# Kernel tuning notes

Hardware: AMD Instinct MI355X
Metric: run time of the kernel (lower is better)

## Reference

```python
import jax, jax.numpy as jnp
import numpy as np

B, L, D, H, FF = 8, 512, 1024, 16, 1024
HD = D // H
EPS = 1e-5
ROPE_BASE = 10000.0
ROPE_DIM = D  # module passes dim=embed_dim (not head_dim) to RotaryPositionalEmbeddings


def _layer_norm(x, g, b):
    m = jnp.mean(x, axis=-1, keepdims=True)
    v = jnp.var(x, axis=-1, keepdims=True)
    return (x - m) * jax.lax.rsqrt(v + EPS) * g + b


def _rope(x):
    # x: [B, H, L, HD]; interleaved-pair rotation, frequencies base**(-2i/ROPE_DIM)
    half = HD // 2
    inv_freq = 1.0 / (ROPE_BASE ** (jnp.arange(half, dtype=jnp.float32) * 2.0 / ROPE_DIM))
    ang = jnp.arange(L, dtype=jnp.float32)[:, None] * inv_freq[None, :]  # [L, half]
    cos = jnp.cos(ang)
    sin = jnp.sin(ang)
    xr = x.reshape(*x.shape[:-1], half, 2)
    x1, x2 = xr[..., 0], xr[..., 1]
    out = jnp.stack([x1 * cos - x2 * sin, x1 * sin + x2 * cos], axis=-1)
    return out.reshape(x.shape).astype(x.dtype)


def setup_inputs() -> dict:
    key = jax.random.key(0)
    ks = jax.random.split(key, 16)
    sd = 0.02
    n = lambda k, shape: (jax.random.normal(k, shape, dtype=jnp.float32) * sd)
    return {
        "input_ids": jax.random.normal(ks[0], (B, L, D), dtype=jnp.float32),
        "Wq": n(ks[1], (FF, D)), "bq": jnp.zeros((D,), jnp.float32),
        "Wk": n(ks[2], (FF, D)), "bk": jnp.zeros((D,), jnp.float32),
        "Wv": n(ks[3], (FF, D)), "bv": jnp.zeros((D,), jnp.float32),
        "Wo": n(ks[4], (D, D)),  "bo": jnp.zeros((D,), jnp.float32),
        "Wf": n(ks[5], (D, FF)), "bf": jnp.zeros((FF,), jnp.float32),
        "g_ffn": jnp.ones((D,), jnp.float32), "b_ffn": jnp.zeros((D,), jnp.float32),
        "g_attn": jnp.ones((FF,), jnp.float32), "b_attn": jnp.zeros((FF,), jnp.float32),
    }


def reference(input_ids, Wq, bq, Wk, bk, Wv, bv, Wo, bo, Wf, bf,
              g_ffn, b_ffn, g_attn, b_attn):
    # FFN branch: computed then DISCARDED in the original source (x is overwritten).
    _ffn_dead = jax.nn.relu(_layer_norm(input_ids, g_ffn, b_ffn) @ Wf + bf)  # noqa: F841

    x = _layer_norm(input_ids, g_attn, b_attn)  # pre_attn_norm applied to input_ids
    q = (x @ Wq + bq).reshape(B, L, H, HD).transpose(0, 2, 1, 3)  # [B,H,L,HD]
    k = (x @ Wk + bk).reshape(B, L, H, HD).transpose(0, 2, 1, 3)
    v = (x @ Wv + bv).reshape(B, L, H, HD).transpose(0, 2, 1, 3)
    q = _rope(q)
    k = _rope(k)

    scale = 1.0 / np.sqrt(HD).astype(np.float32)
    scores = jnp.einsum("bhqd,bhkd->bhqk", q, k) * scale  # [B,H,L,L]
    attn = jax.nn.softmax(scores, axis=-1)
    o = jnp.einsum("bhqk,bhkd->bhqd", attn, v)
    o = o.transpose(0, 2, 1, 3).reshape(B, L, D)
    return input_ids + (o @ Wo + bo)
```

## Files before the change

### kernel.cpp

```cpp
#include <hip/hip_runtime.h>

typedef unsigned short ushort_t;
typedef short bf16x8 __attribute__((ext_vector_type(8)));
typedef float f32x4 __attribute__((ext_vector_type(4)));

#define B_ 8
#define L_ 512
#define D_ 1024
#define H_ 16
#define M_ 4096

__device__ __forceinline__ ushort_t f2bf(float f) {
  union { float f; unsigned u; } v; v.f = f;
  unsigned r = v.u + 0x7FFFu + ((v.u >> 16) & 1u);
  return (ushort_t)(r >> 16);
}

__device__ __forceinline__ void gl_lds16(const ushort_t* g, ushort_t* s) {
  __builtin_amdgcn_global_load_lds((const __attribute__((address_space(1))) void*)(g),
                                   (__attribute__((address_space(3))) void*)(s), 16, 0, 0);
}

__global__ __launch_bounds__(256) void prep_kernel(const float* __restrict__ x,
                                                   const float* __restrict__ g,
                                                   const float* __restrict__ b,
                                                   ushort_t* __restrict__ xn,
                                                   float2* __restrict__ csb,
                                                   const float* __restrict__ w0,
                                                   const float* __restrict__ w1,
                                                   const float* __restrict__ w2,
                                                   const float* __restrict__ w3,
                                                   ushort_t* __restrict__ wt) {
  __shared__ float tile[32][33];
  int blk = blockIdx.x, t = threadIdx.x;
  if (blk < 1024) {
    int row = blk * 4 + (t >> 6);
    int lane = t & 63;
    const float4* xr = (const float4*)(x + (size_t)row * D_);
    float4 v[4];
    float s = 0.f, s2 = 0.f;
#pragma unroll
    for (int j = 0; j < 4; ++j) {
      v[j] = xr[j * 64 + lane];
      s  += v[j].x + v[j].y + v[j].z + v[j].w;
      s2 += v[j].x * v[j].x + v[j].y * v[j].y + v[j].z * v[j].z + v[j].w * v[j].w;
    }
#pragma unroll
    for (int m = 1; m < 64; m <<= 1) { s += __shfl_xor(s, m); s2 += __shfl_xor(s2, m); }
    float mean = s * (1.0f / D_);
    float var  = s2 * (1.0f / D_) - mean * mean;
    float rs   = rsqrtf(var + 1e-5f);
    unsigned long long* outp = (unsigned long long*)(xn + (size_t)row * D_);
#pragma unroll
    for (int j = 0; j < 4; ++j) {
      float4 gg = ((const float4*)g)[j * 64 + lane];
      float4 bb = ((const float4*)b)[j * 64 + lane];
      unsigned long long pk =
          (unsigned long long)f2bf((v[j].x - mean) * rs * gg.x + bb.x)
        | ((unsigned long long)f2bf((v[j].y - mean) * rs * gg.y + bb.y) << 16)
        | ((unsigned long long)f2bf((v[j].z - mean) * rs * gg.z + bb.z) << 32)
        | ((unsigned long long)f2bf((v[j].w - mean) * rs * gg.w + bb.w) << 48);
      outp[j * 64 + lane] = pk;
    }
  } else if (blk < 1088) {
    int idx = (blk - 1024) * 256 + t;
    int l = idx >> 5, i = idx & 31;
    float inv = powf(10000.0f, (-2.0f * (float)i) / 1024.0f);
    float ang = (float)l * inv;
    csb[idx] = make_float2(cosf(ang), sinf(ang));
  } else {
    int wb = blk - 1088;
    int z = wb >> 10;
    const float* W = (z == 0) ? w0 : (z == 1) ? w1 : (z == 2) ? w2 : w3;
    ushort_t* WT = wt + ((size_t)z << 20);
    int rem = wb & 1023;
    int by = rem >> 5, bx = rem & 31;
    int tx = t & 31, ty = t >> 5;
    int k0 = by * 32, n0 = bx * 32;
#pragma unroll
    for (int j = 0; j < 4; ++j)
      tile[ty + 8 * j][tx] = W[(size_t)(k0 + ty + 8 * j) * 1024 + n0 + tx];
    __syncthreads();
#pragma unroll
    for (int j = 0; j < 4; ++j)
      WT[(size_t)(n0 + ty + 8 * j) * 1024 + k0 + tx] = f2bf(tile[tx][ty + 8 * j]);
  }
}

__global__ __launch_bounds__(256) void gemm_qkv_kernel(const ushort_t* __restrict__ xn,
                                                       const ushort_t* __restrict__ wt,
                                                       const float* __restrict__ bq,
                                                       const float* __restrict__ bk,
                                                       const float* __restrict__ bv,
                                                       ushort_t* __restrict__ qb,
                                                       ushort_t* __restrict__ kb,
                                                       ushort_t* __restrict__ vt,
                                                       const float2* __restrict__ csb) {
  __shared__ ushort_t As[64 * 64];
  __shared__ ushort_t Bs[128 * 64];
  int t = threadIdx.x, l = t & 63, w = t >> 6, lr = l & 15, lg = l >> 4;
  int hid = blockIdx.x;
  int xcd = hid & 7, lid = hid >> 3;
  int by = (xcd >> 1) * 16 + lid / 12;
  int bx = (xcd & 1) * 12 + lid % 12;
  int m0 = by * 64;
  int n0g = bx * 128;
  int z = n0g >> 10;
  int n0 = n0g & 1023;
  const float* bias = (z == 0) ? bq : (z == 1) ? bk : bv;
  int wr = w >> 1, wc = w & 1;
  const int sr8 = l >> 3;
  const int scol = ((l & 7) ^ sr8) * 8;

  f32x4 acc[2][4] = {};

  for (int k0 = 0; k0 < 1024; k0 += 64) {
    gl_lds16(&xn[(size_t)(m0 + w * 16 + sr8) * 1024 + k0 + scol], &As[(w * 16) * 64]);
    gl_lds16(&xn[(size_t)(m0 + w * 16 + 8 + sr8) * 1024 + k0 + scol], &As[(w * 16 + 8) * 64]);
    gl_lds16(&wt[(size_t)(n0g + w * 32 + sr8) * 1024 + k0 + scol], &Bs[(w * 32) * 64]);
    gl_lds16(&wt[(size_t)(n0g + w * 32 + 8 + sr8) * 1024 + k0 + scol], &Bs[(w * 32 + 8) * 64]);
    gl_lds16(&wt[(size_t)(n0g + w * 32 + 16 + sr8) * 1024 + k0 + scol], &Bs[(w * 32 + 16) * 64]);
    gl_lds16(&wt[(size_t)(n0g + w * 32 + 24 + sr8) * 1024 + k0 + scol], &Bs[(w * 32 + 24) * 64]);
    __syncthreads();
#pragma unroll
    for (int kk = 0; kk < 2; ++kk) {
      bf16x8 a[2], bfr[4];
#pragma unroll
      for (int mi = 0; mi < 2; ++mi)
        a[mi] = *(const bf16x8*)&As[(wr * 32 + mi * 16 + lr) * 64 + (((kk * 4 + lg) ^ (lr & 7)) << 3)];
#pragma unroll
      for (int ni = 0; ni < 4; ++ni)
        bfr[ni] = *(const bf16x8*)&Bs[(wc * 64 + ni * 16 + lr) * 64 + (((kk * 4 + lg) ^ (lr & 7)) << 3)];
#pragma unroll
      for (int mi = 0; mi < 2; ++mi)
#pragma unroll
        for (int ni = 0; ni < 4; ++ni)
          acc[mi][ni] = __builtin_amdgcn_mfma_f32_16x16x32_bf16(a[mi], bfr[ni], acc[mi][ni], 0, 0, 0);
    }
    __syncthreads();
  }

  if (z < 2) {
    ushort_t* outp = (z == 0) ? qb : kb;
    const float sc = (z == 0) ? 0.18033688f : 1.0f;
#pragma unroll
    for (int mi = 0; mi < 2; ++mi) {
      int rowb = m0 + wr * 32 + mi * 16 + lg * 4;
#pragma unroll
      for (int ni = 0; ni < 4; ++ni) {
        int col = n0 + wc * 64 + ni * 16 + lr;
        float bvv = bias[col];
        int ii = (col & 63) >> 1;
        int codd = col & 1;
#pragma unroll
        for (int r = 0; r < 4; ++r) {
          float val = acc[mi][ni][r] + bvv;
          float par = __shfl_xor(val, 1);
          float2 cs = csb[((rowb + r) & 511) * 32 + ii];
          float y = codd ? (par * cs.y + val * cs.x) : (val * cs.x - par * cs.y);
          outp[(size_t)(rowb + r) * 1024 + col] = f2bf(y * sc);
        }
      }
    }
  } else {
#pragma unroll
    for (int mi = 0; mi < 2; ++mi) {
      int rowb = m0 + wr * 32 + mi * 16 + lg * 4;
      int bidx = rowb >> 9, l0 = rowb & 511;
#pragma unroll
      for (int ni = 0; ni < 4; ++ni) {
        int col = n0 + wc * 64 + ni * 16 + lr;
        float bvv = bias[col];
        unsigned long long pk =
            (unsigned long long)f2bf(acc[mi][ni][0] + bvv)
          | ((unsigned long long)f2bf(acc[mi][ni][1] + bvv) << 16)
          | ((unsigned long long)f2bf(acc[mi][ni][2] + bvv) << 32)
          | ((unsigned long long)f2bf(acc[mi][ni][3] + bvv) << 48);
        *(unsigned long long*)&vt[((size_t)(bidx << 10) + col) * 512 + l0] = pk;
      }
    }
  }
}

__global__ __launch_bounds__(256) void gemm_o_kernel(const ushort_t* __restrict__ A,
                                                     const ushort_t* __restrict__ Bt,
                                                     const float* __restrict__ bias,
                                                     const float* __restrict__ res,
                                                     float* __restrict__ out) {
  __shared__ ushort_t As[64 * 64];
  __shared__ ushort_t Bs[128 * 64];
  int t = threadIdx.x, l = t & 63, w = t >> 6, lr = l & 15, lg = l >> 4;
  int hid = blockIdx.x;
  int lid = (hid & 7) * 64 + (hid >> 3);
  int bx = lid & 7, by = lid >> 3;
  int m0 = by * 64, n0 = bx * 128;
  int wr = w >> 1, wc = w & 1;
  const int srow = l >> 3;
  const int scol = ((l & 7) ^ (srow & 7)) * 8;

  f32x4 acc[2][4] = {};

  for (int k0 = 0; k0 < 1024; k0 += 64) {
#pragma unroll
    for (int i = 0; i < 2; ++i)
      gl_lds16(&A[(size_t)(m0 + w * 16 + i * 8 + srow) * 1024 + k0 + scol],
               &As[(w * 16 + i * 8) * 64]);
#pragma unroll
    for (int i = 0; i < 4; ++i)
      gl_lds16(&Bt[(size_t)(n0 + w * 32 + i * 8 + srow) * 1024 + k0 + scol],
               &Bs[(w * 32 + i * 8) * 64]);
    __syncthreads();
#pragma unroll
    for (int kk = 0; kk < 2; ++kk) {
      bf16x8 a[2], bfr[4];
#pragma unroll
      for (int mi = 0; mi < 2; ++mi)
        a[mi] = *(const bf16x8*)&As[(wr * 32 + mi * 16 + lr) * 64 + (((kk * 4 + lg) ^ (lr & 7)) << 3)];
#pragma unroll
      for (int ni = 0; ni < 4; ++ni)
        bfr[ni] = *(const bf16x8*)&Bs[(wc * 64 + ni * 16 + lr) * 64 + (((kk * 4 + lg) ^ (lr & 7)) << 3)];
#pragma unroll
      for (int mi = 0; mi < 2; ++mi)
#pragma unroll
        for (int ni = 0; ni < 4; ++ni)
          acc[mi][ni] = __builtin_amdgcn_mfma_f32_16x16x32_bf16(a[mi], bfr[ni], acc[mi][ni], 0, 0, 0);
    }
    __syncthreads();
  }

#pragma unroll
  for (int mi = 0; mi < 2; ++mi) {
    int rowb = m0 + wr * 32 + mi * 16 + lg * 4;
#pragma unroll
    for (int ni = 0; ni < 4; ++ni) {
      int col = n0 + wc * 64 + ni * 16 + lr;
      float bvv = bias[col];
#pragma unroll
      for (int r = 0; r < 4; ++r) {
        size_t off = (size_t)(rowb + r) * 1024 + col;
        out[off] = acc[mi][ni][r] + bvv + res[off];
      }
    }
  }
}

__global__ __launch_bounds__(256) void attn_kernel(const ushort_t* __restrict__ q,
                                                   const ushort_t* __restrict__ k,
                                                   const ushort_t* __restrict__ vt,
                                                   ushort_t* __restrict__ o) {
  __shared__ ushort_t Ks[2][64 * 64];
  __shared__ ushort_t Vs[2][64 * 64];
  __shared__ ushort_t Ps[4][2][16 * 64];
  int t = threadIdx.x, l = t & 63, w = t >> 6, lr = l & 15, lg = l >> 4;
  int blk = blockIdx.x;
  int bh = blk & 127, qt = blk >> 7;
  int b = bh >> 4, h = bh & 15;
  const int srow = l >> 3;
  const int scol = ((l & 7) ^ (srow & 7)) * 8;

  bf16x8 qf[2][2];
#pragma unroll
  for (int qm = 0; qm < 2; ++qm) {
    size_t qrow = (size_t)(b * 512 + qt * 128 + w * 32 + qm * 16 + lr);
#pragma unroll
    for (int kh = 0; kh < 2; ++kh)
      qf[qm][kh] = *(const bf16x8*)&q[qrow * 1024 + h * 64 + kh * 32 + lg * 8];
  }

  f32x4 oacc[2][4] = {};
  float lrun[2] = {0.f, 0.f};

#define STAGE(buf, kv0)                                                              \
  {                                                                                  \
    _Pragma("unroll")                                                                \
    for (int j = 0; j < 2; ++j) {                                                    \
      gl_lds16(&k[(size_t)(b * 512 + (kv0) + w * 16 + j * 8 + srow) * 1024 + h * 64 + scol], \
               &Ks[buf][(w * 16 + j * 8) * 64]);                                     \
      gl_lds16(&vt[((size_t)bh * 64 + w * 16 + j * 8 + srow) * 512 + (kv0) + scol],  \
               &Vs[buf][(w * 16 + j * 8) * 64]);                                     \
    }                                                                                \
  }

  STAGE(0, 0);
  __syncthreads();
  int cur = 0;
  for (int it = 0; it < 8; ++it) {
    if (it < 7) { STAGE(cur ^ 1, (it + 1) * 64); }
    bf16x8 kf[2][4];
#pragma unroll
    for (int kh = 0; kh < 2; ++kh)
#pragma unroll
      for (int kn = 0; kn < 4; ++kn)
        kf[kh][kn] = *(const bf16x8*)&Ks[cur][(kn * 16 + lr) * 64 + (((kh * 4 + lg) ^ (lr & 7)) << 3)];

#pragma unroll
    for (int qm = 0; qm < 2; ++qm) {
      f32x4 st[4] = {};
#pragma unroll
      for (int kh = 0; kh < 2; ++kh)
#pragma unroll
        for (int kn = 0; kn < 4; ++kn)
          st[kn] = __builtin_amdgcn_mfma_f32_16x16x32_bf16(kf[kh][kn], qf[qm][kh], st[kn], 0, 0, 0);
      float sm = 0.f;
#pragma unroll
      for (int kn = 0; kn < 4; ++kn) {
        float p0 = exp2f(st[kn][0]);
        float p1 = exp2f(st[kn][1]);
        float p2 = exp2f(st[kn][2]);
        float p3 = exp2f(st[kn][3]);
        sm += p0 + p1 + p2 + p3;
        int kvb = kn * 16 + 4 * lg;
        unsigned long long pk =
            (unsigned long long)f2bf(p0)
          | ((unsigned long long)f2bf(p1) << 16)
          | ((unsigned long long)f2bf(p2) << 32)
          | ((unsigned long long)f2bf(p3) << 48);
        *(unsigned long long*)&Ps[w][qm][lr * 64 + (((kvb >> 3) ^ (lr & 7)) << 3) + (kvb & 7)] = pk;
      }
      sm += __shfl_xor(sm, 16);
      sm += __shfl_xor(sm, 32);
      lrun[qm] += sm;
    }
    asm volatile("s_waitcnt lgkmcnt(0)" ::: "memory");
    __builtin_amdgcn_sched_barrier(0);
#pragma unroll
    for (int kk = 0; kk < 2; ++kk) {
      int sl = (((kk * 4 + lg) ^ (lr & 7)) << 3);
      bf16x8 pb[2];
#pragma unroll
      for (int qm = 0; qm < 2; ++qm)
        pb[qm] = *(const bf16x8*)&Ps[w][qm][lr * 64 + sl];
#pragma unroll
      for (int f = 0; f < 4; ++f) {
        bf16x8 vf = *(const bf16x8*)&Vs[cur][(f * 16 + lr) * 64 + sl];
#pragma unroll
        for (int qm = 0; qm < 2; ++qm)
          oacc[qm][f] = __builtin_amdgcn_mfma_f32_16x16x32_bf16(vf, pb[qm], oacc[qm][f], 0, 0, 0);
      }
    }
    __syncthreads();
    cur ^= 1;
  }
#pragma unroll
  for (int qm = 0; qm < 2; ++qm) {
    float inv = 1.0f / lrun[qm];
    size_t qrow = (size_t)(b * 512 + qt * 128 + w * 32 + qm * 16 + lr);
#pragma unroll
    for (int f = 0; f < 4; ++f) {
      unsigned long long pk =
          (unsigned long long)f2bf(oacc[qm][f][0] * inv)
        | ((unsigned long long)f2bf(oacc[qm][f][1] * inv) << 16)
        | ((unsigned long long)f2bf(oacc[qm][f][2] * inv) << 32)
        | ((unsigned long long)f2bf(oacc[qm][f][3] * inv) << 48);
      *(unsigned long long*)&o[qrow * 1024 + h * 64 + f * 16 + 4 * lg] = pk;
    }
  }
#undef STAGE
}

extern "C" void kernel_launch(void* const* d_in, const int* in_sizes, int n_in,
                              void* d_out, int out_size, void* d_ws, size_t ws_size,
                              hipStream_t stream) {
  const float* input_ids = (const float*)d_in[0];
  const float* Wq = (const float*)d_in[1];
  const float* bq = (const float*)d_in[2];
  const float* Wk = (const float*)d_in[3];
  const float* bk = (const float*)d_in[4];
  const float* Wv = (const float*)d_in[5];
  const float* bv = (const float*)d_in[6];
  const float* Wo = (const float*)d_in[7];
  const float* bo = (const float*)d_in[8];
  const float* g_attn = (const float*)d_in[13];
  const float* b_attn = (const float*)d_in[14];
  float* out = (float*)d_out;

  char* ws = (char*)d_ws;
  const size_t MB = 1024 * 1024;
  ushort_t* wt = (ushort_t*)(ws);
  ushort_t* xn = (ushort_t*)(ws + 8 * MB);
  ushort_t* qb = (ushort_t*)(ws + 16 * MB);
  ushort_t* kb = (ushort_t*)(ws + 24 * MB);
  ushort_t* vt = (ushort_t*)(ws + 32 * MB);
  float2* csb  = (float2*)(ws + 40 * MB);

  prep_kernel<<<5184, 256, 0, stream>>>(input_ids, g_attn, b_attn, xn, csb,
                                        Wq, Wk, Wv, Wo, wt);
  gemm_qkv_kernel<<<1536, 256, 0, stream>>>(xn, wt, bq, bk, bv, qb, kb, vt, csb);
  attn_kernel<<<512, 256, 0, stream>>>(qb, kb, vt, xn);
  gemm_o_kernel<<<512, 256, 0, stream>>>(xn, wt + 3 * MB, bo, input_ids, out);
}
```

Before: 89.27 us.

## Double-buffer B tile in LDS and load A fragments directly into registers

The QKV GEMM now keeps two LDS buffers for the weight tile and prefetches the next K-step's weights with async global-to-LDS loads while computing the current one. The activation operand skips LDS entirely: each wave loads its MFMA A fragments straight from global memory into registers, also one step ahead. This removes the A-tile LDS traffic and one barrier per K-step, and overlaps loads with MFMA work. The cost is more registers and uncoalesced 16-byte global loads for A that rely on cache reuse across the two waves sharing rows.

```diff
diff --git a/kernel.cpp b/kernel.cpp
--- a/kernel.cpp
+++ b/kernel.cpp
@@ -96,8 +96,7 @@
                                                        ushort_t* __restrict__ kb,
                                                        ushort_t* __restrict__ vt,
                                                        const float2* __restrict__ csb) {
-  __shared__ ushort_t As[64 * 64];
-  __shared__ ushort_t Bs[128 * 64];
+  __shared__ ushort_t Bs[2][128 * 64];
   int t = threadIdx.x, l = t & 63, w = t >> 6, lr = l & 15, lg = l >> 4;
   int hid = blockIdx.x;
   int xcd = hid & 7, lid = hid >> 3;
@@ -112,33 +111,63 @@
   const int sr8 = l >> 3;
   const int scol = ((l & 7) ^ sr8) * 8;
 
+  const ushort_t* arow0 = &xn[(size_t)(m0 + wr * 32 + 0 * 16 + lr) * 1024 + lg * 8];
+  const ushort_t* arow1 = &xn[(size_t)(m0 + wr * 32 + 1 * 16 + lr) * 1024 + lg * 8];
+
   f32x4 acc[2][4] = {};
-
-  for (int k0 = 0; k0 < 1024; k0 += 64) {
-    gl_lds16(&xn[(size_t)(m0 + w * 16 + sr8) * 1024 + k0 + scol], &As[(w * 16) * 64]);
-    gl_lds16(&xn[(size_t)(m0 + w * 16 + 8 + sr8) * 1024 + k0 + scol], &As[(w * 16 + 8) * 64]);
-    gl_lds16(&wt[(size_t)(n0g + w * 32 + sr8) * 1024 + k0 + scol], &Bs[(w * 32) * 64]);
-    gl_lds16(&wt[(size_t)(n0g + w * 32 + 8 + sr8) * 1024 + k0 + scol], &Bs[(w * 32 + 8) * 64]);
-    gl_lds16(&wt[(size_t)(n0g + w * 32 + 16 + sr8) * 1024 + k0 + scol], &Bs[(w * 32 + 16) * 64]);
-    gl_lds16(&wt[(size_t)(n0g + w * 32 + 24 + sr8) * 1024 + k0 + scol], &Bs[(w * 32 + 24) * 64]);
-    __syncthreads();
-#pragma unroll
-    for (int kk = 0; kk < 2; ++kk) {
-      bf16x8 a[2], bfr[4];
-#pragma unroll
-      for (int mi = 0; mi < 2; ++mi)
-        a[mi] = *(const bf16x8*)&As[(wr * 32 + mi * 16 + lr) * 64 + (((kk * 4 + lg) ^ (lr & 7)) << 3)];
-#pragma unroll
-      for (int ni = 0; ni < 4; ++ni)
-        bfr[ni] = *(const bf16x8*)&Bs[(wc * 64 + ni * 16 + lr) * 64 + (((kk * 4 + lg) ^ (lr & 7)) << 3)];
-#pragma unroll
-      for (int mi = 0; mi < 2; ++mi)
-#pragma unroll
-        for (int ni = 0; ni < 4; ++ni)
-          acc[mi][ni] = __builtin_amdgcn_mfma_f32_16x16x32_bf16(a[mi], bfr[ni], acc[mi][ni], 0, 0, 0);
-    }
-    __syncthreads();
-  }
+  bf16x8 a0[2][2], a1[2][2];
+
+#pragma unroll
+  for (int kk = 0; kk < 2; ++kk) {
+    a0[kk][0] = *(const bf16x8*)&arow0[kk * 32];
+    a0[kk][1] = *(const bf16x8*)&arow1[kk * 32];
+  }
+  gl_lds16(&wt[(size_t)(n0g + w * 32 + sr8) * 1024 + scol], &Bs[0][(w * 32) * 64]);
+  gl_lds16(&wt[(size_t)(n0g + w * 32 + 8 + sr8) * 1024 + scol], &Bs[0][(w * 32 + 8) * 64]);
+  gl_lds16(&wt[(size_t)(n0g + w * 32 + 16 + sr8) * 1024 + scol], &Bs[0][(w * 32 + 16) * 64]);
+  gl_lds16(&wt[(size_t)(n0g + w * 32 + 24 + sr8) * 1024 + scol], &Bs[0][(w * 32 + 24) * 64]);
+  __syncthreads();
+
+#define KSTEP(AC, AN, BUF, JJ)                                                          \
+  {                                                                                     \
+    if ((JJ) < 15) {                                                                    \
+      int kn = ((JJ) + 1) * 64;                                                         \
+      gl_lds16(&wt[(size_t)(n0g + w * 32 + sr8) * 1024 + kn + scol],                    \
+               &Bs[(BUF) ^ 1][(w * 32) * 64]);                                          \
+      gl_lds16(&wt[(size_t)(n0g + w * 32 + 8 + sr8) * 1024 + kn + scol],                \
+               &Bs[(BUF) ^ 1][(w * 32 + 8) * 64]);                                      \
+      gl_lds16(&wt[(size_t)(n0g + w * 32 + 16 + sr8) * 1024 + kn + scol],               \
+               &Bs[(BUF) ^ 1][(w * 32 + 16) * 64]);                                     \
+      gl_lds16(&wt[(size_t)(n0g + w * 32 + 24 + sr8) * 1024 + kn + scol],               \
+               &Bs[(BUF) ^ 1][(w * 32 + 24) * 64]);                                     \
+      _Pragma("unroll")                                                                 \
+      for (int kk = 0; kk < 2; ++kk) {                                                  \
+        AN[kk][0] = *(const bf16x8*)&arow0[kn + kk * 32];                               \
+        AN[kk][1] = *(const bf16x8*)&arow1[kn + kk * 32];                               \
+      }                                                                                 \
+    }                                                                                   \
+    _Pragma("unroll")                                                                   \
+    for (int kk = 0; kk < 2; ++kk) {                                                    \
+      bf16x8 bfr[4];                                                                    \
+      _Pragma("unroll")                                                                 \
+      for (int ni = 0; ni < 4; ++ni)                                                    \
+        bfr[ni] = *(const bf16x8*)&Bs[BUF][(wc * 64 + ni * 16 + lr) * 64 +              \
+                                           (((kk * 4 + lg) ^ (lr & 7)) << 3)];          \
+      _Pragma("unroll")                                                                 \
+      for (int mi = 0; mi < 2; ++mi)                                                    \
+        _Pragma("unroll")                                                               \
+        for (int ni = 0; ni < 4; ++ni)                                                  \
+          acc[mi][ni] = __builtin_amdgcn_mfma_f32_16x16x32_bf16(AC[kk][mi], bfr[ni],    \
+                                                                acc[mi][ni], 0, 0, 0);  \
+    }                                                                                   \
+    __syncthreads();                                                                    \
+  }
+
+  for (int j = 0; j < 16; j += 2) {
+    KSTEP(a0, a1, 0, j)
+    KSTEP(a1, a0, 1, j + 1)
+  }
+#undef KSTEP
 
   if (z < 2) {
     ushort_t* outp = (z == 0) ? qb : kb;
```

Measured after the change: 116.7 us. 30.7% more time.
